# Kernel optimization log

Measured on AMD Instinct MI355X. Metric: run time of the kernel, lower is better.

## Reference

```python
import jax, jax.numpy as jnp
import numpy as np

DIM = 1024
HEADS = 16
HEAD_DIM = DIM // HEADS
B, N = 4, 4096


def setup_inputs() -> dict:
    key = jax.random.key(0)
    ks = jax.random.split(key, 10)
    s = 1.0 / np.sqrt(DIM)
    return {
        "x": jax.random.normal(ks[0], (B, N, DIM), dtype=jnp.float32),
        "Wq": jax.random.uniform(ks[1], (DIM, DIM), jnp.float32, -s, s),
        "bq": jax.random.uniform(ks[2], (DIM,), jnp.float32, -s, s),
        "Wk": jax.random.uniform(ks[3], (DIM, DIM), jnp.float32, -s, s),
        "bk": jax.random.uniform(ks[4], (DIM,), jnp.float32, -s, s),
        "Wv": jax.random.uniform(ks[5], (DIM, DIM), jnp.float32, -s, s),
        "bv": jax.random.uniform(ks[6], (DIM,), jnp.float32, -s, s),
        "Wo": jax.random.uniform(ks[7], (DIM, DIM), jnp.float32, -s, s),
        "bo": jax.random.uniform(ks[8], (DIM,), jnp.float32, -s, s),
        "stdp": jnp.ones((HEADS,), dtype=jnp.float32),
    }


def reference(x, Wq, bq, Wk, bk, Wv, bv, Wo, bo, stdp):
    b, n, d = x.shape
    h, dh = HEADS, HEAD_DIM
    # projections (torch Linear: x @ W.T + b)
    def proj(W, bias):
        return (x @ W.T + bias).reshape(b, n, h, dh).transpose(0, 2, 1, 3)  # bhnd
    Q = jax.nn.elu(proj(Wq, bq)) + 1.0
    K = jax.nn.elu(proj(Wk, bk)) + 1.0
    V = proj(Wv, bv)
    stdp_w = jax.nn.sigmoid(stdp).reshape(1, h, 1, 1)
    KV = jnp.einsum('bhnd,bhnv->bhdv', K, V)      # (b,h,dh,dh)
    K_sum = K.sum(axis=2)                          # (b,h,dh)
    numerator = jnp.einsum('bhnd,bhdv->bhnv', Q, KV)
    denominator = jnp.einsum('bhnd,bhd->bhn', Q, K_sum)[..., None] + 1e-6
    attn_out = numerator / denominator * stdp_w    # (b,h,n,dh)
    out = attn_out.transpose(0, 2, 1, 3).reshape(b, n, d)
    out = out @ Wo.T + bo
    return (out, jax.lax.stop_gradient(stdp))
```

## Files before the change

### kernel.cpp

```cpp
#include <hip/hip_runtime.h>
#include <hip/hip_bf16.h>

#define DIMSZ 1024
#define SEQLEN 4096
#define NHEAD 16
#define NX 16777216L
#define NW 1048576L

typedef __attribute__((ext_vector_type(8))) short bf16x8;
typedef __attribute__((ext_vector_type(4))) float f32x4;

__device__ __forceinline__ unsigned short f2bf(float f) {
    union { float f; unsigned int i; } c; c.f = f;
    unsigned int x = c.i;
    unsigned int r = (x + 0x7fffu + ((x >> 16) & 1u)) >> 16;
    return (unsigned short)r;
}

__device__ __forceinline__ unsigned int pk2(float lo, float hi) {
    union { float f; unsigned int i; } a, b; a.f = lo; b.f = hi;
    return __builtin_amdgcn_perm(b.i + 0x8000u, a.i + 0x8000u, 0x07060302u);
}

__device__ __forceinline__ void unp4(const unsigned short* p, float* f) {
    uint2 w = *(const uint2*)p;
    union { unsigned int i; float f; } c;
    c.i = w.x << 16;           f[0] = c.f;
    c.i = w.x & 0xffff0000u;   f[1] = c.f;
    c.i = w.y << 16;           f[2] = c.f;
    c.i = w.y & 0xffff0000u;   f[3] = c.f;
}

__device__ __forceinline__ void unp8(const unsigned short* p, float* f) {
    uint4 w = *(const uint4*)p;
    union { unsigned int i; float f; } c;
    c.i = w.x << 16;           f[0] = c.f;
    c.i = w.x & 0xffff0000u;   f[1] = c.f;
    c.i = w.y << 16;           f[2] = c.f;
    c.i = w.y & 0xffff0000u;   f[3] = c.f;
    c.i = w.z << 16;           f[4] = c.f;
    c.i = w.z & 0xffff0000u;   f[5] = c.f;
    c.i = w.w << 16;           f[6] = c.f;
    c.i = w.w & 0xffff0000u;   f[7] = c.f;
}

__device__ __forceinline__ void async16(const void* g, void* l) {
    __builtin_amdgcn_global_load_lds(
        (const __attribute__((address_space(1))) void*)g,
        (__attribute__((address_space(3))) void*)l,
        16, 0, 0);
}

__global__ __launch_bounds__(256) void cast_pack(
    const float* __restrict__ x, const float* __restrict__ Wq,
    const float* __restrict__ Wk, const float* __restrict__ Wv,
    const float* __restrict__ Wo, const float* __restrict__ stdp,
    unsigned short* __restrict__ xb, unsigned short* __restrict__ Wqkv,
    unsigned short* __restrict__ Wob, float* __restrict__ outTail)
{
    long i4 = ((long)blockIdx.x * 256 + threadIdx.x) * 4;
    const float* src; unsigned short* dst; long off;
    if (i4 < NX)               { src = x;  dst = xb;          off = i4; }
    else if (i4 < NX + NW)     { src = Wq; dst = Wqkv;        off = i4 - NX; }
    else if (i4 < NX + 2*NW)   { src = Wk; dst = Wqkv + NW;   off = i4 - NX - NW; }
    else if (i4 < NX + 3*NW)   { src = Wv; dst = Wqkv + 2*NW; off = i4 - NX - 2*NW; }
    else                       { src = Wo; dst = Wob;         off = i4 - NX - 3*NW; }
    float4 v = *(const float4*)(src + off);
    union { unsigned short u[4]; uint2 p; } o;
    o.u[0] = f2bf(v.x); o.u[1] = f2bf(v.y); o.u[2] = f2bf(v.z); o.u[3] = f2bf(v.w);
    *(uint2*)(dst + off) = o.p;
    if (blockIdx.x == 0 && threadIdx.x < NHEAD) outTail[threadIdx.x] = stdp[threadIdx.x];
}

__global__ __launch_bounds__(512, 2) void qkv_gemm8(
    const unsigned short* __restrict__ A, const unsigned short* __restrict__ W,
    const float* __restrict__ bq, const float* __restrict__ bk,
    const float* __restrict__ bv,
    unsigned short* __restrict__ Qb, unsigned short* __restrict__ Kb,
    unsigned short* __restrict__ Vb)
{
    __shared__ __align__(16) char SM[131072];
    const int t = threadIdx.x;
    const int wave = t >> 6, lane = t & 63;
    const int lr = lane & 15, lq = lane >> 4;
    const int wm = wave >> 2, wn = wave & 3;
    const int m0 = blockIdx.x * 256;
    const int c0 = blockIdx.y * 256;

    const int sc = (((t & 7) ^ ((t >> 3) & 7)) * 8);
    const unsigned short* pA = A + (long)(m0 + (t >> 3)) * DIMSZ + sc;
    const unsigned short* pB = W + (long)(c0 + (t >> 3)) * DIMSZ + sc;
    char* ldsW = SM + wave * 1024;

    const int xo = ((lq ^ (lr & 7)) << 4);
    const char* ABase = SM + wm * 16384 + lr * 128;
    const char* BBase = SM + 32768 + (wn * 64 + lr) * 128;

    f32x4 acc[8][4];
    #pragma unroll
    for (int i = 0; i < 8; ++i)
        #pragma unroll
        for (int j = 0; j < 4; ++j) acc[i][j] = (f32x4){0.f, 0.f, 0.f, 0.f};

#define STAGE(Q, O) do {                                                        \
        if ((Q) < 16) {                                                         \
            const int isB_ = ((O) < 2) ? 1 : 0;                                 \
            const int half_ = isB_ ? (O) : ((O) - 2);                           \
            const unsigned short* s_ = (isB_ ? pB : pA)                         \
                                       + (long)half_ * 131072 + (Q) * 64;       \
            char* d_ = ldsW + (((Q) & 1) << 16) + isB_ * 32768 + half_ * 16384; \
            async16(s_, d_);                                                    \
            async16(s_ + 65536, d_ + 8192);                                     \
        }                                                                       \
    } while (0)

    STAGE(0, 0); STAGE(0, 1); STAGE(0, 2); STAGE(0, 3);
    STAGE(1, 0); STAGE(1, 1); STAGE(1, 2);
    asm volatile("s_waitcnt vmcnt(6)" ::: "memory");
    __builtin_amdgcn_s_barrier();

    for (int kt = 0; kt < 16; ++kt) {
        const int buf = (kt & 1) << 16;
        bf16x8 a0[4][2], a1[4][2], bfr[4][2];

        #pragma unroll
        for (int j = 0; j < 4; ++j) {
            bfr[j][0] = *(const bf16x8*)(BBase + buf + j * 2048 + xo);
            bfr[j][1] = *(const bf16x8*)(BBase + buf + j * 2048 + (xo ^ 64));
        }
        #pragma unroll
        for (int i = 0; i < 4; ++i) {
            a0[i][0] = *(const bf16x8*)(ABase + buf + i * 2048 + xo);
            a0[i][1] = *(const bf16x8*)(ABase + buf + i * 2048 + (xo ^ 64));
        }
        STAGE(kt + 1, 3);
        __builtin_amdgcn_s_barrier();
        asm volatile("s_waitcnt lgkmcnt(0)" ::: "memory");
        __builtin_amdgcn_sched_barrier(0);
        __builtin_amdgcn_s_setprio(1);
        #pragma unroll
        for (int s = 0; s < 2; ++s)
            #pragma unroll
            for (int i = 0; i < 4; ++i)
                #pragma unroll
                for (int j = 0; j < 2; ++j)
                    acc[i][j] = __builtin_amdgcn_mfma_f32_16x16x32_bf16(
                        bfr[j][s], a0[i][s], acc[i][j], 0, 0, 0);
        __builtin_amdgcn_s_setprio(0);
        __builtin_amdgcn_s_barrier();

        STAGE(kt + 2, 0);
        __builtin_amdgcn_s_barrier();
        __builtin_amdgcn_s_setprio(1);
        #pragma unroll
        for (int s = 0; s < 2; ++s)
            #pragma unroll
            for (int i = 0; i < 4; ++i)
                #pragma unroll
                for (int j = 2; j < 4; ++j)
                    acc[i][j] = __builtin_amdgcn_mfma_f32_16x16x32_bf16(
                        bfr[j][s], a0[i][s], acc[i][j], 0, 0, 0);
        __builtin_amdgcn_s_setprio(0);
        __builtin_amdgcn_s_barrier();

        #pragma unroll
        for (int i = 0; i < 4; ++i) {
            a1[i][0] = *(const bf16x8*)(ABase + buf + (i + 4) * 2048 + xo);
            a1[i][1] = *(const bf16x8*)(ABase + buf + (i + 4) * 2048 + (xo ^ 64));
        }
        STAGE(kt + 2, 1);
        __builtin_amdgcn_s_barrier();
        asm volatile("s_waitcnt lgkmcnt(0)" ::: "memory");
        __builtin_amdgcn_sched_barrier(0);
        __builtin_amdgcn_s_setprio(1);
        #pragma unroll
        for (int s = 0; s < 2; ++s)
            #pragma unroll
            for (int i = 0; i < 4; ++i)
                #pragma unroll
                for (int j = 0; j < 2; ++j)
                    acc[i + 4][j] = __builtin_amdgcn_mfma_f32_16x16x32_bf16(
                        bfr[j][s], a1[i][s], acc[i + 4][j], 0, 0, 0);
        __builtin_amdgcn_s_setprio(0);
        __builtin_amdgcn_s_barrier();

        STAGE(kt + 2, 2);
        __builtin_amdgcn_s_barrier();
        __builtin_amdgcn_s_setprio(1);
        #pragma unroll
        for (int s = 0; s < 2; ++s)
            #pragma unroll
            for (int i = 0; i < 4; ++i)
                #pragma unroll
                for (int j = 2; j < 4; ++j)
                    acc[i + 4][j] = __builtin_amdgcn_mfma_f32_16x16x32_bf16(
                        bfr[j][s], a1[i][s], acc[i + 4][j], 0, 0, 0);
        __builtin_amdgcn_s_setprio(0);
        if (kt < 14)       asm volatile("s_waitcnt vmcnt(6)" ::: "memory");
        else if (kt == 14) asm volatile("s_waitcnt vmcnt(0)" ::: "memory");
        __builtin_amdgcn_s_barrier();
    }
#undef STAGE

    const int proj = c0 >> 10;
    const float* bias = proj == 0 ? bq : (proj == 1 ? bk : bv);
    const bool qk = proj < 2;
    const int cb = (c0 & 1023) + wn * 64;
    const int q4 = lq * 4;
    #pragma unroll
    for (int j = 0; j < 4; ++j) {
        const float4 b4 = *(const float4*)(bias + cb + 16 * j + q4);
        #pragma unroll
        for (int i = 0; i < 8; ++i) {
            float v0 = acc[i][j][0] + b4.x, v1 = acc[i][j][1] + b4.y;
            float v2 = acc[i][j][2] + b4.z, v3 = acc[i][j][3] + b4.w;
            if (qk) {
                v0 = v0 > 0.f ? v0 + 1.f : __expf(v0);
                v1 = v1 > 0.f ? v1 + 1.f : __expf(v1);
                v2 = v2 > 0.f ? v2 + 1.f : __expf(v2);
                v3 = v3 > 0.f ? v3 + 1.f : __expf(v3);
            }
            const int row = wm * 128 + 16 * i + lr;
            int byte = row * 512 + wn * 128 + j * 32 + q4 * 2;
            byte ^= (row & 7) << 4;
            uint2 pkd; pkd.x = pk2(v0, v1); pkd.y = pk2(v2, v3);
            *(uint2*)(SM + byte) = pkd;
        }
    }
    __syncthreads();
    unsigned short* dstp = proj == 0 ? Qb : (proj == 1 ? Kb : Vb);
    const int colsh = (t & 31) * 8;
    const int h = ((c0 >> 6) + (colsh >> 6)) & 15;
    const int b_ = m0 >> 12;
    unsigned short* dbase = dstp + ((long)(b_ * 16 + h) * SEQLEN) * 64 + (colsh & 63);
    #pragma unroll
    for (int u = 0; u < 16; ++u) {
        const int flat = u * 8192 + t * 16;
        const int row = flat >> 9;
        uint4 val = *(const uint4*)(SM + (flat ^ ((row & 7) << 4)));
        const int n = (m0 + row) & 4095;
        *(uint4*)(dbase + (long)n * 64) = val;
    }
}

__global__ __launch_bounds__(256) void kv_reduce(
    const unsigned short* __restrict__ Kb, const unsigned short* __restrict__ Vb,
    float* __restrict__ KVp, float* __restrict__ Ksump)
{
    __shared__ float red[4096];
    __shared__ float redk[64];
    int bh = blockIdx.x, split = blockIdx.y;
    int t = threadIdx.x;
    int dblk = t & 7, vblk = (t >> 3) & 7, nsub = t >> 6;
    int d0 = dblk * 8, v0 = vblk * 8;
    long rbase = ((long)bh * SEQLEN + split * 256 + nsub * 64) * 64;
    const unsigned short* Kp = Kb + rbase + d0;
    const unsigned short* Vp = Vb + rbase + v0;

    float acc[8][8];
    #pragma unroll
    for (int a = 0; a < 8; ++a)
        #pragma unroll
        for (int c = 0; c < 8; ++c) acc[a][c] = 0.f;
    float ks[8] = {0.f, 0.f, 0.f, 0.f, 0.f, 0.f, 0.f, 0.f};

    for (int i = 0; i < 64; ++i) {
        float kf[8], vf[8];
        unp8(Kp + (long)i * 64, kf);
        unp8(Vp + (long)i * 64, vf);
        if (vblk == 0) {
            #pragma unroll
            for (int d = 0; d < 8; ++d) ks[d] += kf[d];
        }
        #pragma unroll
        for (int vi = 0; vi < 8; ++vi)
            #pragma unroll
            for (int di = 0; di < 8; ++di) acc[vi][di] += vf[vi] * kf[di];
    }

    for (int p = 0; p < 4; ++p) {
        if (nsub == p) {
            #pragma unroll
            for (int vi = 0; vi < 8; ++vi)
                #pragma unroll
                for (int di = 0; di < 8; ++di) {
                    float* a = &red[(v0 + vi) * 64 + d0 + di];
                    if (p == 0) *a = acc[vi][di]; else *a += acc[vi][di];
                }
            if (vblk == 0) {
                #pragma unroll
                for (int di = 0; di < 8; ++di) {
                    float* a = &redk[d0 + di];
                    if (p == 0) *a = ks[di]; else *a += ks[di];
                }
            }
        }
        __syncthreads();
    }

    float* kp = KVp + ((long)split * 64 + bh) * 4096;
    #pragma unroll
    for (int u = 0; u < 4; ++u) {
        int idx = (u * 256 + t) * 4;
        *(float4*)(kp + idx) = *(const float4*)(red + idx);
    }
    if (t < 16)
        *(float4*)(Ksump + ((long)split * 64 + bh) * 64 + t * 4) = *(const float4*)(redk + t * 4);
}

__global__ __launch_bounds__(256) void kv_final(
    const float* __restrict__ KVp, const float* __restrict__ Ksump,
    unsigned short* __restrict__ KVb, float* __restrict__ Ksum)
{
    int bh = blockIdx.x, t = threadIdx.x;
    float s[16];
    #pragma unroll
    for (int g = 0; g < 16; ++g) s[g] = 0.f;
    for (int sp = 0; sp < 16; ++sp) {
        const float* src = KVp + ((long)sp * 64 + bh) * 4096 + t * 16;
        #pragma unroll
        for (int g = 0; g < 4; ++g) {
            float4 v = *(const float4*)(src + g * 4);
            s[g * 4 + 0] += v.x; s[g * 4 + 1] += v.y;
            s[g * 4 + 2] += v.z; s[g * 4 + 3] += v.w;
        }
    }
    uint4 o0, o1;
    o0.x = pk2(s[0], s[1]);  o0.y = pk2(s[2], s[3]);
    o0.z = pk2(s[4], s[5]);  o0.w = pk2(s[6], s[7]);
    o1.x = pk2(s[8], s[9]);  o1.y = pk2(s[10], s[11]);
    o1.z = pk2(s[12], s[13]); o1.w = pk2(s[14], s[15]);
    *(uint4*)(KVb + (long)bh * 4096 + t * 16) = o0;
    *(uint4*)(KVb + (long)bh * 4096 + t * 16 + 8) = o1;
    if (t < 16) {
        float4 a = {0.f, 0.f, 0.f, 0.f};
        for (int p = 0; p < 16; p += 4) {
            #pragma unroll
            for (int q = 0; q < 4; ++q) {
                float4 v = *(const float4*)(Ksump + ((long)(p + q) * 64 + bh) * 64 + t * 4);
                a.x += v.x; a.y += v.y; a.z += v.z; a.w += v.w;
            }
        }
        *(float4*)(Ksum + bh * 64 + t * 4) = a;
    }
}

__global__ __launch_bounds__(256) void attn_kernel(
    const unsigned short* __restrict__ Qb, const unsigned short* __restrict__ KVb,
    const float* __restrict__ Ksum, const float* __restrict__ stdp,
    unsigned short* __restrict__ attn)
{
    __shared__ unsigned short Bsh[64 * 72];
    __shared__ unsigned short Cs[256 * 72];
    __shared__ float ksum_s[64];
    __shared__ float dinv[256];
    int t = threadIdx.x;
    int rc = blockIdx.x;
    int bh = blockIdx.y;
    int b = bh >> 4, h = bh & 15;

    {
        int v = t >> 2, doff = (t & 3) * 16;
        const unsigned short* src = KVb + (long)bh * 4096 + v * 64 + doff;
        *(uint4*)(Bsh + v * 72 + doff)     = *(const uint4*)(src);
        *(uint4*)(Bsh + v * 72 + doff + 8) = *(const uint4*)(src + 8);
        if (t < 64) ksum_s[t] = Ksum[bh * 64 + t];
    }
    __syncthreads();

    int n = rc * 256 + t;
    const unsigned short* qrow = Qb + ((long)bh * SEQLEN + n) * 64;
    float s = 0.f;
    #pragma unroll
    for (int u = 0; u < 64; u += 4) {
        float qf[4]; unp4(qrow + u, qf);
        s += qf[0] * ksum_s[u] + qf[1] * ksum_s[u + 1] + qf[2] * ksum_s[u + 2] + qf[3] * ksum_s[u + 3];
    }
    float sg = 1.f / (1.f + __expf(-stdp[h]));
    dinv[t] = sg / (s + 1e-6f);

    int wave = t >> 6, lane = t & 63, lr = lane & 15, lk = (lane >> 4) * 8;
    int rowbase = rc * 256 + wave * 64;
    f32x4 acc[4][4];
    #pragma unroll
    for (int i = 0; i < 4; ++i)
        #pragma unroll
        for (int j = 0; j < 4; ++j) acc[i][j] = (f32x4){0.f, 0.f, 0.f, 0.f};

    #pragma unroll
    for (int s0 = 0; s0 < 64; s0 += 32) {
        bf16x8 af[4], bfr[4];
        #pragma unroll
        for (int i = 0; i < 4; ++i)
            af[i] = *(const bf16x8*)(Qb + ((long)bh * SEQLEN + rowbase + 16 * i + lr) * 64 + s0 + lk);
        #pragma unroll
        for (int j = 0; j < 4; ++j)
            bfr[j] = *(const bf16x8*)(Bsh + (16 * j + lr) * 72 + s0 + lk);
        #pragma unroll
        for (int i = 0; i < 4; ++i)
            #pragma unroll
            for (int j = 0; j < 4; ++j)
                acc[i][j] = __builtin_amdgcn_mfma_f32_16x16x32_bf16(bfr[j], af[i], acc[i][j], 0, 0, 0);
    }
    __syncthreads();

    int q4 = (lane >> 4) * 4;
    #pragma unroll
    for (int j = 0; j < 4; ++j) {
        int v0c = 16 * j + q4;
        #pragma unroll
        for (int i = 0; i < 4; ++i) {
            int row = wave * 64 + 16 * i + lr;
            float d = dinv[row];
            uint2 pkd;
            pkd.x = pk2(acc[i][j][0] * d, acc[i][j][1] * d);
            pkd.y = pk2(acc[i][j][2] * d, acc[i][j][3] * d);
            *(uint2*)(Cs + row * 72 + v0c) = pkd;
        }
    }
    __syncthreads();
    #pragma unroll
    for (int u = 0; u < 8; ++u) {
        int row = u * 32 + (t >> 3);
        int nn = rc * 256 + row;
        long a = ((long)(b * SEQLEN + nn)) * DIMSZ + h * 64 + (t & 7) * 8;
        *(uint4*)(attn + a) = *(const uint4*)(Cs + row * 72 + (t & 7) * 8);
    }
}

__global__ __launch_bounds__(256) void out_gemm(
    const unsigned short* __restrict__ A, const unsigned short* __restrict__ W,
    const float* __restrict__ bo, float* __restrict__ out)
{
    __shared__ unsigned short As[128 * 32];
    __shared__ unsigned short Bs[128 * 32];
    const int K = DIMSZ;
    int t = threadIdx.x;
    int wave = t >> 6, lane = t & 63;
    int lr = lane & 15, lk = (lane >> 4) * 8;
    int m0 = blockIdx.x * 128;
    int c0 = blockIdx.y * 128;
    int rw = (wave >> 1) * 64, cw = (wave & 1) * 64;

    const unsigned short* Ap = A + (long)(m0 + (t >> 2)) * K + (t & 3) * 8;
    const unsigned short* Wp = W + (long)(c0 + (t >> 2)) * K + (t & 3) * 8;
    char* AsW = (char*)As + wave * 1024;
    char* BsW = (char*)Bs + wave * 1024;

    f32x4 acc[4][4];
    #pragma unroll
    for (int i = 0; i < 4; ++i)
        #pragma unroll
        for (int j = 0; j < 4; ++j) acc[i][j] = (f32x4){0.f, 0.f, 0.f, 0.f};

    for (int k0 = 0; k0 < K; k0 += 32) {
        async16(Ap + k0,          AsW);
        async16(Ap + 64 * K + k0, AsW + 4096);
        async16(Wp + k0,          BsW);
        async16(Wp + 64 * K + k0, BsW + 4096);
        __syncthreads();
        bf16x8 af[4], bfr[4];
        #pragma unroll
        for (int i = 0; i < 4; ++i)
            af[i] = *(const bf16x8*)(As + (rw + 16 * i + lr) * 32 + lk);
        #pragma unroll
        for (int j = 0; j < 4; ++j)
            bfr[j] = *(const bf16x8*)(Bs + (cw + 16 * j + lr) * 32 + lk);
        #pragma unroll
        for (int i = 0; i < 4; ++i)
            #pragma unroll
            for (int j = 0; j < 4; ++j)
                acc[i][j] = __builtin_amdgcn_mfma_f32_16x16x32_bf16(bfr[j], af[i], acc[i][j], 0, 0, 0);
        __syncthreads();
    }

    int q4 = (lane >> 4) * 4;
    #pragma unroll
    for (int j = 0; j < 4; ++j) {
        int c = c0 + cw + 16 * j + q4;
        float4 b4 = *(const float4*)(bo + c);
        #pragma unroll
        for (int i = 0; i < 4; ++i) {
            int gm = m0 + rw + 16 * i + lr;
            float4 v;
            v.x = acc[i][j][0] + b4.x; v.y = acc[i][j][1] + b4.y;
            v.z = acc[i][j][2] + b4.z; v.w = acc[i][j][3] + b4.w;
            *(float4*)(out + (long)gm * DIMSZ + c) = v;
        }
    }
}

extern "C" void kernel_launch(void* const* d_in, const int* in_sizes, int n_in,
                              void* d_out, int out_size, void* d_ws, size_t ws_size,
                              hipStream_t stream) {
    const float* x    = (const float*)d_in[0];
    const float* Wq   = (const float*)d_in[1];
    const float* bq   = (const float*)d_in[2];
    const float* Wk   = (const float*)d_in[3];
    const float* bk   = (const float*)d_in[4];
    const float* Wv   = (const float*)d_in[5];
    const float* bv   = (const float*)d_in[6];
    const float* Wo   = (const float*)d_in[7];
    const float* bo   = (const float*)d_in[8];
    const float* stdp = (const float*)d_in[9];
    float* out = (float*)d_out;

    char* ws = (char*)d_ws;
    unsigned short* xb   = (unsigned short*)(ws);
    float*          KVp  = (float*)(ws);
    unsigned short* attn = (unsigned short*)(ws);
    unsigned short* Wqkv = (unsigned short*)(ws + 33554432L);
    float*          Ksump= (float*)(ws + 33554432L);
    unsigned short* KVb  = (unsigned short*)(ws + 33816576L);
    float*          Ksum = (float*)(ws + 34340864L);
    unsigned short* Wob  = (unsigned short*)(ws + 39845888L);
    unsigned short* Qb   = (unsigned short*)(ws + 41943040L);
    unsigned short* Kb   = (unsigned short*)(ws + 75497472L);
    unsigned short* Vb   = (unsigned short*)(ws + 109051904L);

    cast_pack<<<20480, 256, 0, stream>>>(x, Wq, Wk, Wv, Wo, stdp, xb, Wqkv, Wob,
                                         out + 16777216L);
    qkv_gemm8<<<dim3(64, 12), 512, 0, stream>>>(xb, Wqkv, bq, bk, bv, Qb, Kb, Vb);
    kv_reduce<<<dim3(64, 16), 256, 0, stream>>>(Kb, Vb, KVp, Ksump);
    kv_final<<<64, 256, 0, stream>>>(KVp, Ksump, KVb, Ksum);
    attn_kernel<<<dim3(16, 64), 256, 0, stream>>>(Qb, KVb, Ksum, stdp, attn);
    out_gemm<<<dim3(128, 8), 256, 0, stream>>>(attn, Wob, bo, out);
}
```

Baseline: 358.0 us.

## Replace output GEMM with 256x256 pipelined 8-wave kernel; fuse attn denominator

The output projection GEMM becomes a 512-thread kernel using 256x256 tiles, double-buffered async global-to-LDS loads, XOR-swizzled LDS layout, and interleaved load/MFMA phases with priority hints. This is meant to replace the old 128x128 single-buffered loop, which stalled on a barrier every k-step. The attention kernel now reads KV and Ksum directly from global memory and computes the denominator from the MFMA operand registers, reduced with wave shuffles. That removes the shared-memory staging and one barrier. The risk is occupancy and register pressure from the larger tile, and only 256 blocks to spread across the GPU.

```diff
diff --git a/kernel.cpp b/kernel.cpp
--- a/kernel.cpp
+++ b/kernel.cpp
@@ -20,15 +20,6 @@
 __device__ __forceinline__ unsigned int pk2(float lo, float hi) {
     union { float f; unsigned int i; } a, b; a.f = lo; b.f = hi;
     return __builtin_amdgcn_perm(b.i + 0x8000u, a.i + 0x8000u, 0x07060302u);
-}
-
-__device__ __forceinline__ void unp4(const unsigned short* p, float* f) {
-    uint2 w = *(const uint2*)p;
-    union { unsigned int i; float f; } c;
-    c.i = w.x << 16;           f[0] = c.f;
-    c.i = w.x & 0xffff0000u;   f[1] = c.f;
-    c.i = w.y << 16;           f[2] = c.f;
-    c.i = w.y & 0xffff0000u;   f[3] = c.f;
 }
 
 __device__ __forceinline__ void unp8(const unsigned short* p, float* f) {
@@ -42,6 +33,19 @@
     c.i = w.z & 0xffff0000u;   f[5] = c.f;
     c.i = w.w << 16;           f[6] = c.f;
     c.i = w.w & 0xffff0000u;   f[7] = c.f;
+}
+
+__device__ __forceinline__ void unp8r(bf16x8 v, float* f) {
+    union { bf16x8 s; uint4 w; } u; u.s = v;
+    union { unsigned int i; float f; } c;
+    c.i = u.w.x << 16;           f[0] = c.f;
+    c.i = u.w.x & 0xffff0000u;   f[1] = c.f;
+    c.i = u.w.y << 16;           f[2] = c.f;
+    c.i = u.w.y & 0xffff0000u;   f[3] = c.f;
+    c.i = u.w.z << 16;           f[4] = c.f;
+    c.i = u.w.z & 0xffff0000u;   f[5] = c.f;
+    c.i = u.w.w << 16;           f[6] = c.f;
+    c.i = u.w.w & 0xffff0000u;   f[7] = c.f;
 }
 
 __device__ __forceinline__ void async16(const void* g, void* l) {
@@ -350,42 +354,23 @@
     const float* __restrict__ Ksum, const float* __restrict__ stdp,
     unsigned short* __restrict__ attn)
 {
-    __shared__ unsigned short Bsh[64 * 72];
     __shared__ unsigned short Cs[256 * 72];
-    __shared__ float ksum_s[64];
-    __shared__ float dinv[256];
     int t = threadIdx.x;
     int rc = blockIdx.x;
     int bh = blockIdx.y;
     int b = bh >> 4, h = bh & 15;
 
-    {
-        int v = t >> 2, doff = (t & 3) * 16;
-        const unsigned short* src = KVb + (long)bh * 4096 + v * 64 + doff;
-        *(uint4*)(Bsh + v * 72 + doff)     = *(const uint4*)(src);
-        *(uint4*)(Bsh + v * 72 + doff + 8) = *(const uint4*)(src + 8);
-        if (t < 64) ksum_s[t] = Ksum[bh * 64 + t];
-    }
-    __syncthreads();
-
-    int n = rc * 256 + t;
-    const unsigned short* qrow = Qb + ((long)bh * SEQLEN + n) * 64;
-    float s = 0.f;
-    #pragma unroll
-    for (int u = 0; u < 64; u += 4) {
-        float qf[4]; unp4(qrow + u, qf);
-        s += qf[0] * ksum_s[u] + qf[1] * ksum_s[u + 1] + qf[2] * ksum_s[u + 2] + qf[3] * ksum_s[u + 3];
-    }
-    float sg = 1.f / (1.f + __expf(-stdp[h]));
-    dinv[t] = sg / (s + 1e-6f);
-
     int wave = t >> 6, lane = t & 63, lr = lane & 15, lk = (lane >> 4) * 8;
     int rowbase = rc * 256 + wave * 64;
+    const unsigned short* kvb = KVb + (long)bh * 4096;
+    const float* ksb = Ksum + bh * 64;
+
     f32x4 acc[4][4];
     #pragma unroll
     for (int i = 0; i < 4; ++i)
         #pragma unroll
         for (int j = 0; j < 4; ++j) acc[i][j] = (f32x4){0.f, 0.f, 0.f, 0.f};
+    float ds[4] = {0.f, 0.f, 0.f, 0.f};
 
     #pragma unroll
     for (int s0 = 0; s0 < 64; s0 += 32) {
@@ -395,14 +380,32 @@
             af[i] = *(const bf16x8*)(Qb + ((long)bh * SEQLEN + rowbase + 16 * i + lr) * 64 + s0 + lk);
         #pragma unroll
         for (int j = 0; j < 4; ++j)
-            bfr[j] = *(const bf16x8*)(Bsh + (16 * j + lr) * 72 + s0 + lk);
+            bfr[j] = *(const bf16x8*)(kvb + (16 * j + lr) * 64 + s0 + lk);
+        float4 ka = *(const float4*)(ksb + s0 + lk);
+        float4 kb2 = *(const float4*)(ksb + s0 + lk + 4);
+        float ksf[8] = {ka.x, ka.y, ka.z, ka.w, kb2.x, kb2.y, kb2.z, kb2.w};
+        #pragma unroll
+        for (int i = 0; i < 4; ++i) {
+            float qf[8]; unp8r(af[i], qf);
+            #pragma unroll
+            for (int e = 0; e < 8; ++e) ds[i] += qf[e] * ksf[e];
+        }
         #pragma unroll
         for (int i = 0; i < 4; ++i)
             #pragma unroll
             for (int j = 0; j < 4; ++j)
                 acc[i][j] = __builtin_amdgcn_mfma_f32_16x16x32_bf16(bfr[j], af[i], acc[i][j], 0, 0, 0);
     }
-    __syncthreads();
+
+    float sg = 1.f / (1.f + __expf(-stdp[h]));
+    float dinv_i[4];
+    #pragma unroll
+    for (int i = 0; i < 4; ++i) {
+        float d = ds[i];
+        d += __shfl_xor(d, 16);
+        d += __shfl_xor(d, 32);
+        dinv_i[i] = sg / (d + 1e-6f);
+    }
 
     int q4 = (lane >> 4) * 4;
     #pragma unroll
@@ -411,7 +414,7 @@
         #pragma unroll
         for (int i = 0; i < 4; ++i) {
             int row = wave * 64 + 16 * i + lr;
-            float d = dinv[row];
+            float d = dinv_i[i];
             uint2 pkd;
             pkd.x = pk2(acc[i][j][0] * d, acc[i][j][1] * d);
             pkd.y = pk2(acc[i][j][2] * d, acc[i][j][3] * d);
@@ -428,60 +431,141 @@
     }
 }
 
-__global__ __launch_bounds__(256) void out_gemm(
+__global__ __launch_bounds__(512, 2) void out_gemm8(
     const unsigned short* __restrict__ A, const unsigned short* __restrict__ W,
     const float* __restrict__ bo, float* __restrict__ out)
 {
-    __shared__ unsigned short As[128 * 32];
-    __shared__ unsigned short Bs[128 * 32];
-    const int K = DIMSZ;
-    int t = threadIdx.x;
-    int wave = t >> 6, lane = t & 63;
-    int lr = lane & 15, lk = (lane >> 4) * 8;
-    int m0 = blockIdx.x * 128;
-    int c0 = blockIdx.y * 128;
-    int rw = (wave >> 1) * 64, cw = (wave & 1) * 64;
-
-    const unsigned short* Ap = A + (long)(m0 + (t >> 2)) * K + (t & 3) * 8;
-    const unsigned short* Wp = W + (long)(c0 + (t >> 2)) * K + (t & 3) * 8;
-    char* AsW = (char*)As + wave * 1024;
-    char* BsW = (char*)Bs + wave * 1024;
-
-    f32x4 acc[4][4];
-    #pragma unroll
-    for (int i = 0; i < 4; ++i)
+    __shared__ __align__(16) char SM[131072];
+    const int t = threadIdx.x;
+    const int wave = t >> 6, lane = t & 63;
+    const int lr = lane & 15, lq = lane >> 4;
+    const int wm = wave >> 2, wn = wave & 3;
+    const int m0 = blockIdx.x * 256;
+    const int c0 = blockIdx.y * 256;
+
+    const int sc = (((t & 7) ^ ((t >> 3) & 7)) * 8);
+    const unsigned short* pA = A + (long)(m0 + (t >> 3)) * DIMSZ + sc;
+    const unsigned short* pB = W + (long)(c0 + (t >> 3)) * DIMSZ + sc;
+    char* ldsW = SM + wave * 1024;
+
+    const int xo = ((lq ^ (lr & 7)) << 4);
+    const char* ABase = SM + wm * 16384 + lr * 128;
+    const char* BBase = SM + 32768 + (wn * 64 + lr) * 128;
+
+    f32x4 acc[8][4];
+    #pragma unroll
+    for (int i = 0; i < 8; ++i)
         #pragma unroll
         for (int j = 0; j < 4; ++j) acc[i][j] = (f32x4){0.f, 0.f, 0.f, 0.f};
 
-    for (int k0 = 0; k0 < K; k0 += 32) {
-        async16(Ap + k0,          AsW);
-        async16(Ap + 64 * K + k0, AsW + 4096);
-        async16(Wp + k0,          BsW);
-        async16(Wp + 64 * K + k0, BsW + 4096);
-        __syncthreads();
-        bf16x8 af[4], bfr[4];
-        #pragma unroll
-        for (int i = 0; i < 4; ++i)
-            af[i] = *(const bf16x8*)(As + (rw + 16 * i + lr) * 32 + lk);
-        #pragma unroll
-        for (int j = 0; j < 4; ++j)
-            bfr[j] = *(const bf16x8*)(Bs + (cw + 16 * j + lr) * 32 + lk);
-        #pragma unroll
-        for (int i = 0; i < 4; ++i)
-            #pragma unroll
-            for (int j = 0; j < 4; ++j)
-                acc[i][j] = __builtin_amdgcn_mfma_f32_16x16x32_bf16(bfr[j], af[i], acc[i][j], 0, 0, 0);
-        __syncthreads();
-    }
-
-    int q4 = (lane >> 4) * 4;
+#define STAGE(Q, O) do {                                                        \
+        if ((Q) < 16) {                                                         \
+            const int isB_ = ((O) < 2) ? 1 : 0;                                 \
+            const int half_ = isB_ ? (O) : ((O) - 2);                           \
+            const unsigned short* s_ = (isB_ ? pB : pA)                         \
+                                       + (long)half_ * 131072 + (Q) * 64;       \
+            char* d_ = ldsW + (((Q) & 1) << 16) + isB_ * 32768 + half_ * 16384; \
+            async16(s_, d_);                                                    \
+            async16(s_ + 65536, d_ + 8192);                                     \
+        }                                                                       \
+    } while (0)
+
+    STAGE(0, 0); STAGE(0, 1); STAGE(0, 2); STAGE(0, 3);
+    STAGE(1, 0); STAGE(1, 1); STAGE(1, 2);
+    asm volatile("s_waitcnt vmcnt(6)" ::: "memory");
+    __builtin_amdgcn_s_barrier();
+
+    for (int kt = 0; kt < 16; ++kt) {
+        const int buf = (kt & 1) << 16;
+        bf16x8 a0[4][2], a1[4][2], bfr[4][2];
+
+        #pragma unroll
+        for (int j = 0; j < 4; ++j) {
+            bfr[j][0] = *(const bf16x8*)(BBase + buf + j * 2048 + xo);
+            bfr[j][1] = *(const bf16x8*)(BBase + buf + j * 2048 + (xo ^ 64));
+        }
+        #pragma unroll
+        for (int i = 0; i < 4; ++i) {
+            a0[i][0] = *(const bf16x8*)(ABase + buf + i * 2048 + xo);
+            a0[i][1] = *(const bf16x8*)(ABase + buf + i * 2048 + (xo ^ 64));
+        }
+        STAGE(kt + 1, 3);
+        __builtin_amdgcn_s_barrier();
+        asm volatile("s_waitcnt lgkmcnt(0)" ::: "memory");
+        __builtin_amdgcn_sched_barrier(0);
+        __builtin_amdgcn_s_setprio(1);
+        #pragma unroll
+        for (int s = 0; s < 2; ++s)
+            #pragma unroll
+            for (int i = 0; i < 4; ++i)
+                #pragma unroll
+                for (int j = 0; j < 2; ++j)
+                    acc[i][j] = __builtin_amdgcn_mfma_f32_16x16x32_bf16(
+                        bfr[j][s], a0[i][s], acc[i][j], 0, 0, 0);
+        __builtin_amdgcn_s_setprio(0);
+        __builtin_amdgcn_s_barrier();
+
+        STAGE(kt + 2, 0);
+        __builtin_amdgcn_s_barrier();
+        __builtin_amdgcn_s_setprio(1);
+        #pragma unroll
+        for (int s = 0; s < 2; ++s)
+            #pragma unroll
+            for (int i = 0; i < 4; ++i)
+                #pragma unroll
+                for (int j = 2; j < 4; ++j)
+                    acc[i][j] = __builtin_amdgcn_mfma_f32_16x16x32_bf16(
+                        bfr[j][s], a0[i][s], acc[i][j], 0, 0, 0);
+        __builtin_amdgcn_s_setprio(0);
+        __builtin_amdgcn_s_barrier();
+
+        #pragma unroll
+        for (int i = 0; i < 4; ++i) {
+            a1[i][0] = *(const bf16x8*)(ABase + buf + (i + 4) * 2048 + xo);
+            a1[i][1] = *(const bf16x8*)(ABase + buf + (i + 4) * 2048 + (xo ^ 64));
+        }
+        STAGE(kt + 2, 1);
+        __builtin_amdgcn_s_barrier();
+        asm volatile("s_waitcnt lgkmcnt(0)" ::: "memory");
+        __builtin_amdgcn_sched_barrier(0);
+        __builtin_amdgcn_s_setprio(1);
+        #pragma unroll
+        for (int s = 0; s < 2; ++s)
+            #pragma unroll
+            for (int i = 0; i < 4; ++i)
+                #pragma unroll
+                for (int j = 0; j < 2; ++j)
+                    acc[i + 4][j] = __builtin_amdgcn_mfma_f32_16x16x32_bf16(
+                        bfr[j][s], a1[i][s], acc[i + 4][j], 0, 0, 0);
+        __builtin_amdgcn_s_setprio(0);
+        __builtin_amdgcn_s_barrier();
+
+        STAGE(kt + 2, 2);
+        __builtin_amdgcn_s_barrier();
+        __builtin_amdgcn_s_setprio(1);
+        #pragma unroll
+        for (int s = 0; s < 2; ++s)
+            #pragma unroll
+            for (int i = 0; i < 4; ++i)
+                #pragma unroll
+                for (int j = 2; j < 4; ++j)
+                    acc[i + 4][j] = __builtin_amdgcn_mfma_f32_16x16x32_bf16(
+                        bfr[j][s], a1[i][s], acc[i + 4][j], 0, 0, 0);
+        __builtin_amdgcn_s_setprio(0);
+        if (kt < 14)       asm volatile("s_waitcnt vmcnt(6)" ::: "memory");
+        else if (kt == 14) asm volatile("s_waitcnt vmcnt(0)" ::: "memory");
+        __builtin_amdgcn_s_barrier();
+    }
+#undef STAGE
+
+    const int q4 = lq * 4;
     #pragma unroll
     for (int j = 0; j < 4; ++j) {
-        int c = c0 + cw + 16 * j + q4;
-        float4 b4 = *(const float4*)(bo + c);
-        #pragma unroll
-        for (int i = 0; i < 4; ++i) {
-            int gm = m0 + rw + 16 * i + lr;
+        const int c = c0 + wn * 64 + 16 * j + q4;
+        const float4 b4 = *(const float4*)(bo + c);
+        #pragma unroll
+        for (int i = 0; i < 8; ++i) {
+            const int gm = m0 + wm * 128 + 16 * i + lr;
             float4 v;
             v.x = acc[i][j][0] + b4.x; v.y = acc[i][j][1] + b4.y;
             v.z = acc[i][j][2] + b4.z; v.w = acc[i][j][3] + b4.w;
@@ -524,5 +608,5 @@
     kv_reduce<<<dim3(64, 16), 256, 0, stream>>>(Kb, Vb, KVp, Ksump);
     kv_final<<<64, 256, 0, stream>>>(KVp, Ksump, KVb, Ksum);
     attn_kernel<<<dim3(16, 64), 256, 0, stream>>>(Qb, KVb, Ksum, stdp, attn);
-    out_gemm<<<dim3(128, 8), 256, 0, stream>>>(attn, Wob, bo, out);
-}
+    out_gemm8<<<dim3(64, 4), 512, 0, stream>>>(attn, Wob, bo, out);
+}
```

New measurement: 345.7 us. 3.4% less time.
